# Kernel tuning notes

Hardware: AMD Instinct MI355X
Metric: run time of the kernel (lower is better)

## Reference

```python
import jax, jax.numpy as jnp
import numpy as np

N_LEVELS = 7
N_HEADS = 2
HIDDEN = 128
LP_P = 4.0  # LPPool1d norm


def setup_inputs() -> dict:
    key = jax.random.key(0)
    ks = jax.random.split(key, 9)
    B, S, H = 2048, 200, HIDDEN
    item_seq = jax.random.randint(ks[0], (B, S), 0, 100)
    item_seq_emb = jax.random.normal(ks[1], (B, S, H), dtype=jnp.float32)
    item_seq_len = jax.random.randint(ks[2], (B,), 0, S)
    scale = 0.02
    W_lq = jax.random.normal(ks[3], (H, H), dtype=jnp.float32) * scale
    b_lq = jnp.zeros((H,), dtype=jnp.float32)
    Wq = jax.random.normal(ks[4], (H, H), dtype=jnp.float32) * scale
    bq = jnp.zeros((H,), dtype=jnp.float32)
    Wk = jax.random.normal(ks[5], (H, H), dtype=jnp.float32) * scale
    bk = jnp.zeros((H,), dtype=jnp.float32)
    return {"item_seq": item_seq, "item_seq_emb": item_seq_emb,
            "item_seq_len": item_seq_len, "W_lq": W_lq, "b_lq": b_lq,
            "Wq": Wq, "bq": bq, "Wk": Wk, "bk": bk}


def reference(item_seq, item_seq_emb, item_seq_len, W_lq, b_lq, Wq, bq, Wk, bk):
    B, S, H = item_seq_emb.shape
    nh, L = N_HEADS, N_LEVELS
    d = H // nh
    mask = item_seq > 0  # [B,S]

    # multi-level gather of last j+1 positions; torch clamp(-1) + index -1 == last pos
    j = jnp.arange(L)
    idx = jnp.clip(item_seq_len[:, None] - (j[None, :] + 1), -1, 1000)  # [B,L]
    idx = jnp.where(idx < 0, idx + S, idx)
    gathered = jnp.take_along_axis(item_seq_emb, idx[:, :, None], axis=1)  # [B,L,H]
    level_emb = jnp.cumsum(gathered, axis=1)  # level i = sum of gathers 0..i

    # shared level-query linear (ModuleList([lin]*L) aliases one Linear)
    queries = level_emb @ W_lq.T + b_lq  # [B,L,H]

    # raw torch .view() reshapes replicated exactly
    q = (queries @ Wq.T + bq).reshape(B * nh, L, d)
    k = (item_seq_emb @ Wk.T + bk).reshape(B * nh, S, d)
    v = item_seq_emb.reshape(B, S, nh, d)

    alpha = jax.nn.sigmoid(jnp.einsum('bld,bsd->bls', q, k))  # [B*nh, L, S]
    alpha = alpha.reshape(B, nh * L, S).transpose(0, 2, 1)  # [B, S, nh*L]
    alpha = jax.nn.softmax(alpha, axis=1)

    # LPPool1d(p=4, kernel=L, stride=L) over last dim -> [B,S,nh]
    alpha = alpha.reshape(B, S, nh, L)
    alpha = jnp.sum(alpha ** LP_P, axis=-1) ** (1.0 / LP_P)

    alpha = jnp.where(mask[:, :, None], alpha, -jnp.inf)
    alpha = jax.nn.softmax(alpha, axis=1)  # dropout off (inference)

    weighted = (alpha[..., None] * v).reshape(B, S, H) * mask[:, :, None].astype(item_seq_emb.dtype)
    return jnp.sum(weighted, axis=1)  # [B,H]
```

## Files before the change

### kernel.cpp

```cpp
#include <hip/hip_runtime.h>
#include <hip/hip_bf16.h>

#define SEQ 200
#define HID 128
#define NLVL 7

#define WS_M16_W 0
#define WS_BF    32768
#define WS_VB    33280
#define WS_CB    33792
#define WS_WC    33796
#define WS_BC    50180
#define WS_WORDS 50308

typedef __attribute__((ext_vector_type(8))) short short8;
typedef __attribute__((ext_vector_type(4))) float f32x4;

__device__ __forceinline__ float bf_lo(unsigned u) { return __uint_as_float(u << 16); }
__device__ __forceinline__ float bf_hi(unsigned u) { return __uint_as_float(u & 0xffff0000u); }
__device__ __forceinline__ unsigned short bf_bits(float f) {
    __hip_bfloat16 h = __float2bfloat16(f);
    return *reinterpret_cast<unsigned short*>(&h);
}
__device__ __forceinline__ unsigned pack_bf(float a, float b) {
    return (unsigned)bf_bits(a) | ((unsigned)bf_bits(b) << 16);
}

__global__ __launch_bounds__(256) void precomp0(
    const float* __restrict__ Wlq, const float* __restrict__ blq,
    const float* __restrict__ Wq,  const float* __restrict__ bq,
    float* __restrict__ ws)
{
    int id = blockIdx.x * 256 + threadIdx.x;
    int r = id >> 7, j = id & 127;
    float acc = 0.f;
    #pragma unroll 8
    for (int c = 0; c < 128; ++c) acc += Wq[r * 128 + c] * Wlq[c * 128 + j];
    ws[WS_WC + id] = acc;
    if (id < 128) {
        float b = bq[id];
        #pragma unroll 8
        for (int c = 0; c < 128; ++c) b += Wq[id * 128 + c] * blq[c];
        ws[WS_BC + id] = b;
    }
}

__global__ __launch_bounds__(256) void precomp1(
    const float* __restrict__ Wk, const float* __restrict__ bk, float* __restrict__ ws)
{
    int gid = blockIdx.x * 256 + threadIdx.x;
    if (gid < 65536) {
        int j = gid & 127, c = (gid >> 7) & 127, g = gid >> 14;
        int u = g >> 1, par = g & 1;
        const float* wc = ws + WS_WC + u * 64 * 128 + j;
        const float* wk = Wk + par * 64 * 128 + c;
        float acc = 0.f;
        #pragma unroll 8
        for (int d = 0; d < 64; ++d) acc += wc[d * 128] * wk[d * 128];
        ((__hip_bfloat16*)ws)[gid] = __float2bfloat16(acc);
    } else if (gid < 66048) {
        int t = gid - 65536, c = t & 127, g = t >> 7;
        int u = g >> 1, par = g & 1;
        float acc = 0.f;
        #pragma unroll 8
        for (int d = 0; d < 64; ++d)
            acc += ws[WS_BC + u * 64 + d] * Wk[(par * 64 + d) * 128 + c];
        ws[WS_BF + t] = acc;
    } else if (gid < 66560) {
        int t = gid - 66048, j = t & 127, g = t >> 7;
        int u = g >> 1, par = g & 1;
        float acc = 0.f;
        #pragma unroll 8
        for (int d = 0; d < 64; ++d)
            acc += ws[WS_WC + (u * 64 + d) * 128 + j] * bk[par * 64 + d];
        ws[WS_VB + t] = acc;
    } else if (gid < 66564) {
        int g = gid - 66560, u = g >> 1, par = g & 1;
        float acc = 0.f;
        for (int d = 0; d < 64; ++d)
            acc += ws[WS_BC + u * 64 + d] * bk[par * 64 + d];
        ws[WS_CB + g] = acc;
    }
}

__global__ __launch_bounds__(512, 8) void mixer_main(
    const int* __restrict__ item_seq,
    const float* __restrict__ emb,
    const int* __restrict__ seq_len,
    const float* __restrict__ ws,
    float* __restrict__ out)
{
    const int b    = blockIdx.x;
    const int tid  = threadIdx.x;
    const int wave = tid >> 6, lane = tid & 63;

    __shared__ __align__(16) short s_qkhi[30 * 136];
    __shared__ __align__(16) short s_qklo[30 * 136];
    __shared__ __align__(16) char  s_region[14 * 208 * 4];
    __shared__ float s_qb[28];
    __shared__ float s_rinv[14];
    __shared__ __align__(16) float s_A[2 * SEQ];
    __shared__ __align__(16) float s_red[512];

    float* s_scores = (float*)s_region;
    float* s_lvl    = (float*)s_region;
    short* s_lvl16  = (short*)(s_region + 3584);

    const float* embb = emb + (size_t)b * SEQ * HID;

    if (tid < HID) {
        const int len = seq_len[b];
        float e[NLVL];
        #pragma unroll
        for (int j = 0; j < NLVL; ++j) {
            int idx = len - (j + 1);
            if (idx < 0) idx = SEQ - 1;
            e[j] = embb[(size_t)idx * HID + tid];
        }
        float acc = 0.f;
        #pragma unroll
        for (int j = 0; j < NLVL; ++j) {
            acc += e[j];
            s_lvl[j * HID + tid] = acc;
            s_lvl16[j * 136 + tid] = (short)bf_bits(acc);
        }
    } else if (tid < 196) {
        int t = tid - 128;
        ((uint2*)(s_qkhi + 28 * 136))[t] = make_uint2(0u, 0u);
        ((uint2*)(s_qklo + 28 * 136))[t] = make_uint2(0u, 0u);
    }
    __syncthreads();

    {
        const int g = wave >> 1, halfm = wave & 1;
        const int mrow = lane & 15, quad = lane >> 4;
        short8 bfrag[4];
        #pragma unroll
        for (int k = 0; k < 4; ++k)
            bfrag[k] = *(const short8*)(s_lvl16 + mrow * 136 + k * 32 + quad * 8);
        const short* M16 = (const short*)ws;
        #pragma unroll
        for (int mt = 0; mt < 4; ++mt) {
            int mtile = halfm * 4 + mt;
            int cbase = mtile * 16 + quad * 4;
            f32x4 acc;
            #pragma unroll
            for (int r = 0; r < 4; ++r) acc[r] = ws[WS_BF + g * 128 + cbase + r];
            const short* Ab = M16 + (g * 128 + mtile * 16 + mrow) * 128;
            #pragma unroll
            for (int k = 0; k < 4; ++k) {
                short8 afrag = *(const short8*)(Ab + k * 32 + quad * 8);
                acc = __builtin_amdgcn_mfma_f32_16x16x32_bf16(afrag, bfrag[k], acc, 0, 0, 0);
            }
            if (mrow < NLVL) {
                int qrow = mrow * 4 + g;
                unsigned h01 = pack_bf(acc[0], acc[1]);
                unsigned h23 = pack_bf(acc[2], acc[3]);
                float l0 = acc[0] - bf_lo(h01), l1 = acc[1] - bf_hi(h01);
                float l2 = acc[2] - bf_lo(h23), l3 = acc[3] - bf_hi(h23);
                *(uint2*)(s_qkhi + qrow * 136 + cbase) = make_uint2(h01, h23);
                *(uint2*)(s_qklo + qrow * 136 + cbase) = make_uint2(pack_bf(l0, l1), pack_bf(l2, l3));
            }
        }
        if (tid < 28) {
            int qrow = tid, gg = qrow & 3, L = qrow >> 2;
            const float* vb = ws + WS_VB + gg * 128;
            const float* lv = s_lvl + L * 128;
            float acc = ws[WS_CB + gg];
            #pragma unroll 8
            for (int j = 0; j < 128; ++j) acc += lv[j] * vb[j];
            s_qb[qrow] = acc;
        }
    }
    __syncthreads();

    {
        const int ln = lane & 15, quad = lane >> 4;
        #pragma unroll 1
        for (int t = wave; t < 14; t += 8) {
            const int h = t / 7, mtile = t % 7;
            int gqrow = mtile * 16 + ln;
            int rowg = h * 100 + (gqrow < 100 ? gqrow : 99);
            const float* Arow = embb + (size_t)rowg * HID;
            float qbv = (ln < 14) ? s_qb[h * 14 + ln] : 0.f;
            f32x4 acc;
            acc[0] = qbv; acc[1] = qbv; acc[2] = qbv; acc[3] = qbv;
            #pragma unroll 2
            for (int kk = 0; kk < 4; ++kk) {
                float4 v0 = *(const float4*)(Arow + kk * 32 + quad * 8);
                float4 v1 = *(const float4*)(Arow + kk * 32 + quad * 8 + 4);
                short8 afrag;
                afrag[0] = (short)bf_bits(v0.x); afrag[1] = (short)bf_bits(v0.y);
                afrag[2] = (short)bf_bits(v0.z); afrag[3] = (short)bf_bits(v0.w);
                afrag[4] = (short)bf_bits(v1.x); afrag[5] = (short)bf_bits(v1.y);
                afrag[6] = (short)bf_bits(v1.z); afrag[7] = (short)bf_bits(v1.w);
                const int boff = (h * 14 + ln) * 136 + kk * 32 + quad * 8;
                short8 bhi = *(const short8*)(s_qkhi + boff);
                short8 blo = *(const short8*)(s_qklo + boff);
                acc = __builtin_amdgcn_mfma_f32_16x16x32_bf16(afrag, bhi, acc, 0, 0, 0);
                acc = __builtin_amdgcn_mfma_f32_16x16x32_bf16(afrag, blo, acc, 0, 0, 0);
            }
            if (ln < 14) {
                int srow = (h * 7 + (ln >> 1)) * 208;
                int par = ln & 1;
                #pragma unroll
                for (int i = 0; i < 4; ++i) {
                    int gq = mtile * 16 + quad * 4 + i;
                    if (gq < 100)
                        s_scores[srow + 2 * gq + par] = 1.f / (1.f + __expf(-acc[i]));
                }
            }
        }
    }
    __syncthreads();

    for (int rr = wave; rr < 14; rr += 8) {
        const float* row = s_scores + rr * 208;
        float e0 = __expf(row[lane]);
        float e1 = __expf(row[lane + 64]);
        float e2 = __expf(row[lane + 128]);
        float e3 = (lane + 192 < 200) ? __expf(row[lane + 192]) : 0.f;
        float sum = e0 + e1 + e2 + e3;
        #pragma unroll
        for (int mm = 1; mm < 64; mm <<= 1) sum += __shfl_xor(sum, mm, 64);
        if (lane == 0) s_rinv[rr] = 1.f / sum;
    }
    __syncthreads();

    if (tid < 2 * SEQ) {
        int h = tid / SEQ, s2 = tid % SEQ;
        float ssum = 0.f;
        #pragma unroll
        for (int l = 0; l < NLVL; ++l) {
            float v = __expf(s_scores[(h * NLVL + l) * 208 + s2]) * s_rinv[h * NLVL + l];
            float v2 = v * v;
            ssum += v2 * v2;
        }
        float A = sqrtf(sqrtf(ssum));
        int m = item_seq[(size_t)b * SEQ + s2];
        s_A[tid] = (m > 0) ? __expf(A) : 0.f;
    }
    __syncthreads();

    {
        int c = tid & 127, qq = tid >> 7;
        int h = c >> 6;
        const float* wv = s_A + h * SEQ + qq * 50;
        const float* eg = embb + (size_t)(qq * 50) * HID + c;
        float acc = 0.f;
        #pragma unroll 10
        for (int s = 0; s < 50; ++s)
            acc += wv[s] * eg[(size_t)s * HID];
        s_red[tid] = acc;
    }
    __syncthreads();

    if (tid < HID) {
        int h = tid >> 6;
        const float* row = s_A + h * SEQ;
        float sum = row[lane] + row[lane + 64] + row[lane + 128]
                  + ((lane + 192 < 200) ? row[lane + 192] : 0.f);
        #pragma unroll
        for (int mm = 1; mm < 64; mm <<= 1) sum += __shfl_xor(sum, mm, 64);
        float inv = 1.f / sum;
        float tot = (s_red[tid] + s_red[tid + 128] + s_red[tid + 256] + s_red[tid + 384]) * inv;
        out[(size_t)b * HID + tid] = tot;
    }
}

__global__ __launch_bounds__(256) void mixer_fallback(
    const int* __restrict__ item_seq, const float* __restrict__ emb,
    const int* __restrict__ seq_len,
    const float* __restrict__ Wlq, const float* __restrict__ blq,
    const float* __restrict__ Wq,  const float* __restrict__ bq,
    const float* __restrict__ Wk,  const float* __restrict__ bk,
    float* __restrict__ out)
{
    const int b = blockIdx.x, tid = threadIdx.x;
    __shared__ unsigned s_embu[SEQ * 65];
    __shared__ float s_qk[28 * 128];
    __shared__ float s_qb[28];
    __shared__ float s_tmp[2800];
    __shared__ float s_A[400];
    __shared__ float s_red[256];
    __shared__ float s_inv[2];

    {
        const float4* src = (const float4*)(emb + (size_t)b * SEQ * HID);
        for (int i = tid; i < SEQ * 32; i += 256) {
            int row = i >> 5, j = i & 31;
            float4 v = src[i];
            unsigned* dst = s_embu + row * 65 + 2 * j;
            dst[0] = pack_bf(v.x, v.y);
            dst[1] = pack_bf(v.z, v.w);
        }
    }
    const int len = seq_len[b];
    if (tid < HID) {
        float acc = 0.f;
        for (int j = 0; j < NLVL; ++j) {
            int idx = len - (j + 1);
            if (idx < 0) idx = SEQ - 1;
            acc += emb[(size_t)b * SEQ * HID + (size_t)idx * HID + tid];
            s_tmp[j * HID + tid] = acc;
        }
    }
    __syncthreads();
    for (int t = tid; t < NLVL * HID; t += 256) {
        int l = t >> 7, c = t & 127;
        const float* x = s_tmp + l * HID;
        float acc = blq[c];
        #pragma unroll 8
        for (int k = 0; k < HID; ++k) acc += x[k] * Wlq[c * HID + k];
        s_tmp[896 + t] = acc;
    }
    __syncthreads();
    for (int t = tid; t < NLVL * HID; t += 256) {
        int l = t >> 7, c = t & 127;
        const float* x = s_tmp + 896 + l * HID;
        float acc = bq[c];
        #pragma unroll 8
        for (int k = 0; k < HID; ++k) acc += x[k] * Wq[c * HID + k];
        s_tmp[t] = acc;
    }
    __syncthreads();
    for (int o = tid; o < 28 * 128; o += 256) {
        int qrow = o >> 7, c = o & 127;
        int hl = qrow >> 1, par = qrow & 1;
        const float* qv = s_tmp + hl * 64;
        float acc = 0.f;
        #pragma unroll 8
        for (int d2 = 0; d2 < 64; ++d2) acc += qv[d2] * Wk[(par * 64 + d2) * HID + c];
        s_qk[qrow * 128 + c] = acc;
    }
    if (tid < 28) {
        int hl = tid >> 1, par = tid & 1;
        float acc = 0.f;
        for (int d2 = 0; d2 < 64; ++d2) acc += s_tmp[hl * 64 + d2] * bk[par * 64 + d2];
        s_qb[tid] = acc;
    }
    __syncthreads();
    for (int o = tid; o < 700; o += 256) {
        int hl = o / 50, g = o % 50;
        int h = (hl >= 7) ? 1 : 0;
        int rA = h * 100 + g, rB = rA + 50;
        const unsigned* eA = s_embu + rA * 65;
        const unsigned* eB = s_embu + rB * 65;
        const float* k0 = s_qk + (hl * 2) * 128;
        const float* k1 = s_qk + (hl * 2 + 1) * 128;
        float a0 = 0.f, a1 = 0.f, c0a = 0.f, c1a = 0.f;
        #pragma unroll 4
        for (int kk = 0; kk < 64; ++kk) {
            unsigned uA = eA[kk], uB = eB[kk];
            float2 w0 = *(const float2*)(k0 + 2 * kk);
            float2 w1 = *(const float2*)(k1 + 2 * kk);
            float alo = bf_lo(uA), ahi = bf_hi(uA);
            float blo = bf_lo(uB), bhi = bf_hi(uB);
            a0 += alo * w0.x + ahi * w0.y;  a1 += alo * w1.x + ahi * w1.y;
            c0a += blo * w0.x + bhi * w0.y; c1a += blo * w1.x + bhi * w1.y;
        }
        float qb0 = s_qb[hl * 2], qb1 = s_qb[hl * 2 + 1];
        float* row = s_tmp + hl * 200;
        row[2 * g]       = 1.f / (1.f + __expf(-(a0 + qb0)));
        row[2 * g + 1]   = 1.f / (1.f + __expf(-(a1 + qb1)));
        row[2 * g + 100] = 1.f / (1.f + __expf(-(c0a + qb0)));
        row[2 * g + 101] = 1.f / (1.f + __expf(-(c1a + qb1)));
    }
    __syncthreads();
    const int wave = tid >> 6, lane = tid & 63;
    for (int r = wave; r < 14; r += 4) {
        float* row = s_tmp + r * 200;
        float e0 = __expf(row[lane]), e1 = __expf(row[lane + 64]);
        float e2 = __expf(row[lane + 128]);
        float e3 = (lane + 192 < 200) ? __expf(row[lane + 192]) : 0.f;
        float sum = e0 + e1 + e2 + e3;
        #pragma unroll
        for (int m = 1; m < 64; m <<= 1) sum += __shfl_xor(sum, m, 64);
        float inv = 1.f / sum;
        row[lane] = e0 * inv; row[lane + 64] = e1 * inv; row[lane + 128] = e2 * inv;
        if (lane + 192 < 200) row[lane + 192] = e3 * inv;
    }
    __syncthreads();
    for (int o = tid; o < 2 * SEQ; o += 256) {
        int h = o / SEQ, s2 = o % SEQ;
        float ssum = 0.f;
        #pragma unroll
        for (int l = 0; l < NLVL; ++l) {
            float v = s_tmp[(h * NLVL + l) * 200 + s2];
            float v2 = v * v; ssum += v2 * v2;
        }
        float A = sqrtf(sqrtf(ssum));
        s_A[o] = (item_seq[(size_t)b * SEQ + s2] > 0) ? __expf(A) : 0.f;
    }
    __syncthreads();
    if (wave < 2) {
        const float* row = s_A + wave * SEQ;
        float sum = row[lane] + row[lane + 64] + row[lane + 128]
                  + ((lane + 192 < 200) ? row[lane + 192] : 0.f);
        #pragma unroll
        for (int m = 1; m < 64; m <<= 1) sum += __shfl_xor(sum, m, 64);
        if (lane == 0) s_inv[wave] = 1.f / sum;
    }
    __syncthreads();
    {
        int c = tid & 127, halfb = tid >> 7;
        int h = c >> 6;
        const float* wv = s_A + h * SEQ + halfb * 100;
        float acc = 0.f;
        #pragma unroll 4
        for (int s2 = 0; s2 < 100; ++s2) {
            unsigned u = s_embu[(halfb * 100 + s2) * 65 + (c >> 1)];
            acc += wv[s2] * ((c & 1) ? bf_hi(u) : bf_lo(u));
        }
        s_red[tid] = acc;
    }
    __syncthreads();
    if (tid < HID) {
        int h = tid >> 6;
        out[(size_t)b * HID + tid] = (s_red[tid] + s_red[tid + 128]) * s_inv[h];
    }
}

extern "C" void kernel_launch(void* const* d_in, const int* in_sizes, int n_in,
                              void* d_out, int out_size, void* d_ws, size_t ws_size,
                              hipStream_t stream) {
    const int* item_seq = (const int*)d_in[0];
    const float* emb    = (const float*)d_in[1];
    const int* seq_len  = (const int*)d_in[2];
    const float* Wlq    = (const float*)d_in[3];
    const float* blq    = (const float*)d_in[4];
    const float* Wq     = (const float*)d_in[5];
    const float* bq     = (const float*)d_in[6];
    const float* Wk     = (const float*)d_in[7];
    const float* bk     = (const float*)d_in[8];
    float* out          = (float*)d_out;
    const int B = in_sizes[2];

    if (ws_size >= (size_t)WS_WORDS * 4) {
        float* ws = (float*)d_ws;
        precomp0<<<64, 256, 0, stream>>>(Wlq, blq, Wq, bq, ws);
        precomp1<<<261, 256, 0, stream>>>(Wk, bk, ws);
        mixer_main<<<B, 512, 0, stream>>>(item_seq, emb, seq_len, ws, out);
    } else {
        mixer_fallback<<<B, 256, 0, stream>>>(item_seq, emb, seq_len, Wlq, blq, Wq, bq, Wk, bk, out);
    }
}
```

Baseline: 358.8 us.

## Prefetch score-GEMM embedding tiles before query projection to overlap global loads

The embedding rows for each wave's score-tile MFMA are now loaded from global memory and converted to bf16 at kernel start, before the first barrier. This hides that load latency behind the level gather and query-projection phases. The tile loop is replaced by at most two statically assigned tiles held in registers. The score row stride changes from 208 to 212 to alter LDS bank mapping, and launch bounds drop from 8 to 6 waves per EU. The extra live registers may lower occupancy.

```diff
diff --git a/kernel.cpp b/kernel.cpp
--- a/kernel.cpp
+++ b/kernel.cpp
@@ -12,6 +12,8 @@
 #define WS_WC    33796
 #define WS_BC    50180
 #define WS_WORDS 50308
+
+#define SCST 212
 
 typedef __attribute__((ext_vector_type(8))) short short8;
 typedef __attribute__((ext_vector_type(4))) float f32x4;
@@ -83,7 +85,7 @@
     }
 }
 
-__global__ __launch_bounds__(512, 8) void mixer_main(
+__global__ __launch_bounds__(512, 6) void mixer_main(
     const int* __restrict__ item_seq,
     const float* __restrict__ emb,
     const int* __restrict__ seq_len,
@@ -93,10 +95,11 @@
     const int b    = blockIdx.x;
     const int tid  = threadIdx.x;
     const int wave = tid >> 6, lane = tid & 63;
+    const int ln   = lane & 15, quad = lane >> 4;
 
     __shared__ __align__(16) short s_qkhi[30 * 136];
     __shared__ __align__(16) short s_qklo[30 * 136];
-    __shared__ __align__(16) char  s_region[14 * 208 * 4];
+    __shared__ __align__(16) char  s_region[14 * SCST * 4];
     __shared__ float s_qb[28];
     __shared__ float s_rinv[14];
     __shared__ __align__(16) float s_A[2 * SEQ];
@@ -108,8 +111,25 @@
 
     const float* embb = emb + (size_t)b * SEQ * HID;
 
+    const int t0 = wave;
+    const int t1 = (wave >= 2) ? wave + 6 : -1;
+
+    const int len = seq_len[b];
+
+    float4 p[8];
+    {
+        const int h = t0 / 7, m = t0 % 7;
+        int gq = m * 16 + ln;
+        int rowg = h * 100 + (gq < 100 ? gq : 99);
+        const float* Ar = embb + (size_t)rowg * HID + quad * 8;
+        #pragma unroll
+        for (int kk = 0; kk < 4; ++kk) {
+            p[2 * kk]     = *(const float4*)(Ar + kk * 32);
+            p[2 * kk + 1] = *(const float4*)(Ar + kk * 32 + 4);
+        }
+    }
+
     if (tid < HID) {
-        const int len = seq_len[b];
         float e[NLVL];
         #pragma unroll
         for (int j = 0; j < NLVL; ++j) {
@@ -129,11 +149,42 @@
         ((uint2*)(s_qkhi + 28 * 136))[t] = make_uint2(0u, 0u);
         ((uint2*)(s_qklo + 28 * 136))[t] = make_uint2(0u, 0u);
     }
+
+    short8 a0[4], a1[4];
+    #pragma unroll
+    for (int kk = 0; kk < 4; ++kk) {
+        short8 f;
+        f[0] = (short)bf_bits(p[2*kk].x); f[1] = (short)bf_bits(p[2*kk].y);
+        f[2] = (short)bf_bits(p[2*kk].z); f[3] = (short)bf_bits(p[2*kk].w);
+        f[4] = (short)bf_bits(p[2*kk+1].x); f[5] = (short)bf_bits(p[2*kk+1].y);
+        f[6] = (short)bf_bits(p[2*kk+1].z); f[7] = (short)bf_bits(p[2*kk+1].w);
+        a0[kk] = f;
+    }
+    if (t1 >= 0) {
+        const int h = t1 / 7, m = t1 % 7;
+        int gq = m * 16 + ln;
+        int rowg = h * 100 + (gq < 100 ? gq : 99);
+        const float* Ar = embb + (size_t)rowg * HID + quad * 8;
+        #pragma unroll
+        for (int kk = 0; kk < 4; ++kk) {
+            p[2 * kk]     = *(const float4*)(Ar + kk * 32);
+            p[2 * kk + 1] = *(const float4*)(Ar + kk * 32 + 4);
+        }
+        #pragma unroll
+        for (int kk = 0; kk < 4; ++kk) {
+            short8 f;
+            f[0] = (short)bf_bits(p[2*kk].x); f[1] = (short)bf_bits(p[2*kk].y);
+            f[2] = (short)bf_bits(p[2*kk].z); f[3] = (short)bf_bits(p[2*kk].w);
+            f[4] = (short)bf_bits(p[2*kk+1].x); f[5] = (short)bf_bits(p[2*kk+1].y);
+            f[6] = (short)bf_bits(p[2*kk+1].z); f[7] = (short)bf_bits(p[2*kk+1].w);
+            a1[kk] = f;
+        }
+    }
     __syncthreads();
 
     {
         const int g = wave >> 1, halfm = wave & 1;
-        const int mrow = lane & 15, quad = lane >> 4;
+        const int mrow = ln;
         short8 bfrag[4];
         #pragma unroll
         for (int k = 0; k < 4; ++k)
@@ -174,48 +225,38 @@
     }
     __syncthreads();
 
-    {
-        const int ln = lane & 15, quad = lane >> 4;
-        #pragma unroll 1
-        for (int t = wave; t < 14; t += 8) {
-            const int h = t / 7, mtile = t % 7;
-            int gqrow = mtile * 16 + ln;
-            int rowg = h * 100 + (gqrow < 100 ? gqrow : 99);
-            const float* Arow = embb + (size_t)rowg * HID;
-            float qbv = (ln < 14) ? s_qb[h * 14 + ln] : 0.f;
-            f32x4 acc;
-            acc[0] = qbv; acc[1] = qbv; acc[2] = qbv; acc[3] = qbv;
-            #pragma unroll 2
-            for (int kk = 0; kk < 4; ++kk) {
-                float4 v0 = *(const float4*)(Arow + kk * 32 + quad * 8);
-                float4 v1 = *(const float4*)(Arow + kk * 32 + quad * 8 + 4);
-                short8 afrag;
-                afrag[0] = (short)bf_bits(v0.x); afrag[1] = (short)bf_bits(v0.y);
-                afrag[2] = (short)bf_bits(v0.z); afrag[3] = (short)bf_bits(v0.w);
-                afrag[4] = (short)bf_bits(v1.x); afrag[5] = (short)bf_bits(v1.y);
-                afrag[6] = (short)bf_bits(v1.z); afrag[7] = (short)bf_bits(v1.w);
-                const int boff = (h * 14 + ln) * 136 + kk * 32 + quad * 8;
-                short8 bhi = *(const short8*)(s_qkhi + boff);
-                short8 blo = *(const short8*)(s_qklo + boff);
-                acc = __builtin_amdgcn_mfma_f32_16x16x32_bf16(afrag, bhi, acc, 0, 0, 0);
-                acc = __builtin_amdgcn_mfma_f32_16x16x32_bf16(afrag, blo, acc, 0, 0, 0);
+    #pragma unroll
+    for (int which = 0; which < 2; ++which) {
+        const int t = (which == 0) ? t0 : t1;
+        if (t < 0) continue;
+        const int h = t / 7, mtile = t % 7;
+        const short8* af = (which == 0) ? a0 : a1;
+        float qbv = (ln < 14) ? s_qb[h * 14 + ln] : 0.f;
+        f32x4 acc;
+        acc[0] = qbv; acc[1] = qbv; acc[2] = qbv; acc[3] = qbv;
+        #pragma unroll
+        for (int kk = 0; kk < 4; ++kk) {
+            const int boff = (h * 14 + ln) * 136 + kk * 32 + quad * 8;
+            short8 bhi = *(const short8*)(s_qkhi + boff);
+            short8 blo = *(const short8*)(s_qklo + boff);
+            acc = __builtin_amdgcn_mfma_f32_16x16x32_bf16(af[kk], bhi, acc, 0, 0, 0);
+            acc = __builtin_amdgcn_mfma_f32_16x16x32_bf16(af[kk], blo, acc, 0, 0, 0);
+        }
+        if (ln < 14) {
+            int srow = (h * 7 + (ln >> 1)) * SCST;
+            int par = ln & 1;
+            #pragma unroll
+            for (int i = 0; i < 4; ++i) {
+                int gq = mtile * 16 + quad * 4 + i;
+                if (gq < 100)
+                    s_scores[srow + 2 * gq + par] = 1.f / (1.f + __expf(-acc[i]));
             }
-            if (ln < 14) {
-                int srow = (h * 7 + (ln >> 1)) * 208;
-                int par = ln & 1;
-                #pragma unroll
-                for (int i = 0; i < 4; ++i) {
-                    int gq = mtile * 16 + quad * 4 + i;
-                    if (gq < 100)
-                        s_scores[srow + 2 * gq + par] = 1.f / (1.f + __expf(-acc[i]));
-                }
-            }
         }
     }
     __syncthreads();
 
     for (int rr = wave; rr < 14; rr += 8) {
-        const float* row = s_scores + rr * 208;
+        const float* row = s_scores + rr * SCST;
         float e0 = __expf(row[lane]);
         float e1 = __expf(row[lane + 64]);
         float e2 = __expf(row[lane + 128]);
@@ -232,7 +273,7 @@
         float ssum = 0.f;
         #pragma unroll
         for (int l = 0; l < NLVL; ++l) {
-            float v = __expf(s_scores[(h * NLVL + l) * 208 + s2]) * s_rinv[h * NLVL + l];
+            float v = __expf(s_scores[(h * NLVL + l) * SCST + s2]) * s_rinv[h * NLVL + l];
             float v2 = v * v;
             ssum += v2 * v2;
         }
```

New measurement: 391.8 us. 1.09x slower.

## Prefetch score-GEMM rows early, fuse softmax denominators into score epilogue

Applied to the files above, without the earlier changes.

Each wave now loads and converts its first embedding tile for the score MFMA before the level/query stage and its barrier, hiding global latency behind that work. The second score tile is issued early and unrolled. The softmax row sums are accumulated during the sigmoid epilogue with shuffles and LDS atomics, which removes a separate reduction pass and one barrier. The per-level query-bias dot product is split across 16 lanes with shuffle reduction. The score stride is padded to 212. The cost is higher register pressure and LDS atomic contention on the denominators.

```diff
diff --git a/kernel.cpp b/kernel.cpp
--- a/kernel.cpp
+++ b/kernel.cpp
@@ -13,6 +13,8 @@
 #define WS_BC    50180
 #define WS_WORDS 50308
 
+#define SCST 212
+
 typedef __attribute__((ext_vector_type(8))) short short8;
 typedef __attribute__((ext_vector_type(4))) float f32x4;
 
@@ -24,6 +26,14 @@
 }
 __device__ __forceinline__ unsigned pack_bf(float a, float b) {
     return (unsigned)bf_bits(a) | ((unsigned)bf_bits(b) << 16);
+}
+__device__ __forceinline__ short8 cvt8(float4 a, float4 b) {
+    short8 f;
+    f[0] = (short)bf_bits(a.x); f[1] = (short)bf_bits(a.y);
+    f[2] = (short)bf_bits(a.z); f[3] = (short)bf_bits(a.w);
+    f[4] = (short)bf_bits(b.x); f[5] = (short)bf_bits(b.y);
+    f[6] = (short)bf_bits(b.z); f[7] = (short)bf_bits(b.w);
+    return f;
 }
 
 __global__ __launch_bounds__(256) void precomp0(
@@ -93,12 +103,13 @@
     const int b    = blockIdx.x;
     const int tid  = threadIdx.x;
     const int wave = tid >> 6, lane = tid & 63;
+    const int ln   = lane & 15, quad = lane >> 4;
 
     __shared__ __align__(16) short s_qkhi[30 * 136];
     __shared__ __align__(16) short s_qklo[30 * 136];
-    __shared__ __align__(16) char  s_region[14 * 208 * 4];
+    __shared__ __align__(16) char  s_region[14 * SCST * 4];
     __shared__ float s_qb[28];
-    __shared__ float s_rinv[14];
+    __shared__ float s_denom[14];
     __shared__ __align__(16) float s_A[2 * SEQ];
     __shared__ __align__(16) float s_red[512];
 
@@ -108,8 +119,25 @@
 
     const float* embb = emb + (size_t)b * SEQ * HID;
 
+    const int len = seq_len[b];
+
+    const int hA = wave / 7, mA = wave % 7;
+    const float* Ar0;
+    {
+        int gq = mA * 16 + ln;
+        int rowg = hA * 100 + (gq < 100 ? gq : 99);
+        Ar0 = embb + (size_t)rowg * HID + quad * 8;
+    }
+    float4 q0 = *(const float4*)(Ar0);
+    float4 q1 = *(const float4*)(Ar0 + 4);
+    float4 q2 = *(const float4*)(Ar0 + 32);
+    float4 q3 = *(const float4*)(Ar0 + 36);
+    float4 q4 = *(const float4*)(Ar0 + 64);
+    float4 q5 = *(const float4*)(Ar0 + 68);
+    float4 q6 = *(const float4*)(Ar0 + 96);
+    float4 q7 = *(const float4*)(Ar0 + 100);
+
     if (tid < HID) {
-        const int len = seq_len[b];
         float e[NLVL];
         #pragma unroll
         for (int j = 0; j < NLVL; ++j) {
@@ -128,12 +156,19 @@
         int t = tid - 128;
         ((uint2*)(s_qkhi + 28 * 136))[t] = make_uint2(0u, 0u);
         ((uint2*)(s_qklo + 28 * 136))[t] = make_uint2(0u, 0u);
-    }
+    } else if (tid < 210) {
+        s_denom[tid - 196] = 0.f;
+    }
+
+    short8 a00 = cvt8(q0, q1);
+    short8 a01 = cvt8(q2, q3);
+    short8 a02 = cvt8(q4, q5);
+    short8 a03 = cvt8(q6, q7);
     __syncthreads();
 
     {
         const int g = wave >> 1, halfm = wave & 1;
-        const int mrow = lane & 15, quad = lane >> 4;
+        const int mrow = ln;
         short8 bfrag[4];
         #pragma unroll
         for (int k = 0; k < 4; ++k)
@@ -162,68 +197,110 @@
                 *(uint2*)(s_qklo + qrow * 136 + cbase) = make_uint2(pack_bf(l0, l1), pack_bf(l2, l3));
             }
         }
-        if (tid < 28) {
-            int qrow = tid, gg = qrow & 3, L = qrow >> 2;
+        if (tid < 448) {
+            int grp = tid >> 4, sub = tid & 15;
+            int gg = grp & 3, L = grp >> 2;
             const float* vb = ws + WS_VB + gg * 128;
             const float* lv = s_lvl + L * 128;
-            float acc = ws[WS_CB + gg];
-            #pragma unroll 8
-            for (int j = 0; j < 128; ++j) acc += lv[j] * vb[j];
-            s_qb[qrow] = acc;
+            float acc = 0.f;
+            #pragma unroll
+            for (int k = 0; k < 8; ++k) {
+                int j = sub + 16 * k;
+                acc += lv[j] * vb[j];
+            }
+            acc += __shfl_xor(acc, 1, 16);
+            acc += __shfl_xor(acc, 2, 16);
+            acc += __shfl_xor(acc, 4, 16);
+            acc += __shfl_xor(acc, 8, 16);
+            if (sub == 0) s_qb[grp] = acc + ws[WS_CB + gg];
         }
     }
     __syncthreads();
 
     {
-        const int ln = lane & 15, quad = lane >> 4;
-        #pragma unroll 1
-        for (int t = wave; t < 14; t += 8) {
-            const int h = t / 7, mtile = t % 7;
-            int gqrow = mtile * 16 + ln;
-            int rowg = h * 100 + (gqrow < 100 ? gqrow : 99);
-            const float* Arow = embb + (size_t)rowg * HID;
-            float qbv = (ln < 14) ? s_qb[h * 14 + ln] : 0.f;
+        const bool hasB = (wave < 6);
+        const int mB = wave + 1;
+        const float* ArB = embb;
+        float4 r0, r1, r2, r3;
+        if (hasB) {
+            int gq = mB * 16 + ln;
+            int rowg = 100 + (gq < 100 ? gq : 99);
+            ArB = embb + (size_t)rowg * HID + quad * 8;
+            r0 = *(const float4*)(ArB);
+            r1 = *(const float4*)(ArB + 4);
+            r2 = *(const float4*)(ArB + 32);
+            r3 = *(const float4*)(ArB + 36);
+        }
+        {
+            float qbv = (ln < 14) ? s_qb[hA * 14 + ln] : 0.f;
             f32x4 acc;
             acc[0] = qbv; acc[1] = qbv; acc[2] = qbv; acc[3] = qbv;
-            #pragma unroll 2
-            for (int kk = 0; kk < 4; ++kk) {
-                float4 v0 = *(const float4*)(Arow + kk * 32 + quad * 8);
-                float4 v1 = *(const float4*)(Arow + kk * 32 + quad * 8 + 4);
-                short8 afrag;
-                afrag[0] = (short)bf_bits(v0.x); afrag[1] = (short)bf_bits(v0.y);
-                afrag[2] = (short)bf_bits(v0.z); afrag[3] = (short)bf_bits(v0.w);
-                afrag[4] = (short)bf_bits(v1.x); afrag[5] = (short)bf_bits(v1.y);
-                afrag[6] = (short)bf_bits(v1.z); afrag[7] = (short)bf_bits(v1.w);
-                const int boff = (h * 14 + ln) * 136 + kk * 32 + quad * 8;
-                short8 bhi = *(const short8*)(s_qkhi + boff);
-                short8 blo = *(const short8*)(s_qklo + boff);
-                acc = __builtin_amdgcn_mfma_f32_16x16x32_bf16(afrag, bhi, acc, 0, 0, 0);
-                acc = __builtin_amdgcn_mfma_f32_16x16x32_bf16(afrag, blo, acc, 0, 0, 0);
-            }
+            const int bb = (hA * 14 + ln) * 136 + quad * 8;
+            acc = __builtin_amdgcn_mfma_f32_16x16x32_bf16(a00, *(const short8*)(s_qkhi + bb), acc, 0, 0, 0);
+            acc = __builtin_amdgcn_mfma_f32_16x16x32_bf16(a00, *(const short8*)(s_qklo + bb), acc, 0, 0, 0);
+            acc = __builtin_amdgcn_mfma_f32_16x16x32_bf16(a01, *(const short8*)(s_qkhi + bb + 32), acc, 0, 0, 0);
+            acc = __builtin_amdgcn_mfma_f32_16x16x32_bf16(a01, *(const short8*)(s_qklo + bb + 32), acc, 0, 0, 0);
+            acc = __builtin_amdgcn_mfma_f32_16x16x32_bf16(a02, *(const short8*)(s_qkhi + bb + 64), acc, 0, 0, 0);
+            acc = __builtin_amdgcn_mfma_f32_16x16x32_bf16(a02, *(const short8*)(s_qklo + bb + 64), acc, 0, 0, 0);
+            acc = __builtin_amdgcn_mfma_f32_16x16x32_bf16(a03, *(const short8*)(s_qkhi + bb + 96), acc, 0, 0, 0);
+            acc = __builtin_amdgcn_mfma_f32_16x16x32_bf16(a03, *(const short8*)(s_qklo + bb + 96), acc, 0, 0, 0);
+            float part = 0.f;
             if (ln < 14) {
-                int srow = (h * 7 + (ln >> 1)) * 208;
-                int par = ln & 1;
+                int srow = (hA * 7 + (ln >> 1)) * SCST, par = ln & 1;
                 #pragma unroll
                 for (int i = 0; i < 4; ++i) {
-                    int gq = mtile * 16 + quad * 4 + i;
-                    if (gq < 100)
-                        s_scores[srow + 2 * gq + par] = 1.f / (1.f + __expf(-acc[i]));
+                    int gq = mA * 16 + quad * 4 + i;
+                    if (gq < 100) {
+                        float sg = 1.f / (1.f + __expf(-acc[i]));
+                        s_scores[srow + 2 * gq + par] = sg;
+                        part += __expf(sg);
+                    }
                 }
             }
-        }
-    }
-    __syncthreads();
-
-    for (int rr = wave; rr < 14; rr += 8) {
-        const float* row = s_scores + rr * 208;
-        float e0 = __expf(row[lane]);
-        float e1 = __expf(row[lane + 64]);
-        float e2 = __expf(row[lane + 128]);
-        float e3 = (lane + 192 < 200) ? __expf(row[lane + 192]) : 0.f;
-        float sum = e0 + e1 + e2 + e3;
-        #pragma unroll
-        for (int mm = 1; mm < 64; mm <<= 1) sum += __shfl_xor(sum, mm, 64);
-        if (lane == 0) s_rinv[rr] = 1.f / sum;
+            part += __shfl_xor(part, 16, 64);
+            part += __shfl_xor(part, 32, 64);
+            if (ln < 14 && quad == 0)
+                atomicAdd(&s_denom[hA * 7 + (ln >> 1)], part);
+        }
+        if (hasB) {
+            short8 b0 = cvt8(r0, r1);
+            short8 b1 = cvt8(r2, r3);
+            float4 r4 = *(const float4*)(ArB + 64);
+            float4 r5 = *(const float4*)(ArB + 68);
+            float4 r6 = *(const float4*)(ArB + 96);
+            float4 r7 = *(const float4*)(ArB + 100);
+            float qbv = (ln < 14) ? s_qb[14 + ln] : 0.f;
+            f32x4 acc;
+            acc[0] = qbv; acc[1] = qbv; acc[2] = qbv; acc[3] = qbv;
+            const int bb = (14 + ln) * 136 + quad * 8;
+            acc = __builtin_amdgcn_mfma_f32_16x16x32_bf16(b0, *(const short8*)(s_qkhi + bb), acc, 0, 0, 0);
+            acc = __builtin_amdgcn_mfma_f32_16x16x32_bf16(b0, *(const short8*)(s_qklo + bb), acc, 0, 0, 0);
+            acc = __builtin_amdgcn_mfma_f32_16x16x32_bf16(b1, *(const short8*)(s_qkhi + bb + 32), acc, 0, 0, 0);
+            acc = __builtin_amdgcn_mfma_f32_16x16x32_bf16(b1, *(const short8*)(s_qklo + bb + 32), acc, 0, 0, 0);
+            short8 b2 = cvt8(r4, r5);
+            short8 b3 = cvt8(r6, r7);
+            acc = __builtin_amdgcn_mfma_f32_16x16x32_bf16(b2, *(const short8*)(s_qkhi + bb + 64), acc, 0, 0, 0);
+            acc = __builtin_amdgcn_mfma_f32_16x16x32_bf16(b2, *(const short8*)(s_qklo + bb + 64), acc, 0, 0, 0);
+            acc = __builtin_amdgcn_mfma_f32_16x16x32_bf16(b3, *(const short8*)(s_qkhi + bb + 96), acc, 0, 0, 0);
+            acc = __builtin_amdgcn_mfma_f32_16x16x32_bf16(b3, *(const short8*)(s_qklo + bb + 96), acc, 0, 0, 0);
+            float part = 0.f;
+            if (ln < 14) {
+                int srow = (7 + (ln >> 1)) * SCST, par = ln & 1;
+                #pragma unroll
+                for (int i = 0; i < 4; ++i) {
+                    int gq = mB * 16 + quad * 4 + i;
+                    if (gq < 100) {
+                        float sg = 1.f / (1.f + __expf(-acc[i]));
+                        s_scores[srow + 2 * gq + par] = sg;
+                        part += __expf(sg);
+                    }
+                }
+            }
+            part += __shfl_xor(part, 16, 64);
+            part += __shfl_xor(part, 32, 64);
+            if (ln < 14 && quad == 0)
+                atomicAdd(&s_denom[7 + (ln >> 1)], part);
+        }
     }
     __syncthreads();
 
@@ -232,7 +309,8 @@
         float ssum = 0.f;
         #pragma unroll
         for (int l = 0; l < NLVL; ++l) {
-            float v = __expf(s_scores[(h * NLVL + l) * 208 + s2]) * s_rinv[h * NLVL + l];
+            float v = __fdividef(__expf(s_scores[(h * NLVL + l) * SCST + s2]),
+                                 s_denom[h * NLVL + l]);
             float v2 = v * v;
             ssum += v2 * v2;
         }
```

New measurement: 364.1 us. Within noise of the previous version (+1.5%).

## Split per-batch query projection into separate kernel and fuse softmax exp into scoring

Applied to the files above, without the earlier changes.

Moves the per-batch level gather and query/key-combined projection into a new precomp2 kernel that writes hi/lo bf16 query tiles and biases to workspace, which mixer_main then bulk-copies into LDS. The exponent for the first softmax is now computed in the score epilogue, with row sums accumulated through shared atomics instead of a separate reduction pass. This is meant to shorten the main kernel's serial prologue and drop one barrier-delimited phase. In exchange it adds a kernel launch, a global round trip of about 16KB per batch, and requires a much larger workspace, falling back to the slow path otherwise.

```diff
diff --git a/kernel.cpp b/kernel.cpp
--- a/kernel.cpp
+++ b/kernel.cpp
@@ -13,6 +13,11 @@
 #define WS_BC    50180
 #define WS_WORDS 50308
 
+#define WS_QK    51200
+#define QK_STRIDE 4112
+
+#define SCST 212
+
 typedef __attribute__((ext_vector_type(8))) short short8;
 typedef __attribute__((ext_vector_type(4))) float f32x4;
 
@@ -24,6 +29,14 @@
 }
 __device__ __forceinline__ unsigned pack_bf(float a, float b) {
     return (unsigned)bf_bits(a) | ((unsigned)bf_bits(b) << 16);
+}
+__device__ __forceinline__ short8 cvt8(float4 a, float4 b) {
+    short8 f;
+    f[0] = (short)bf_bits(a.x); f[1] = (short)bf_bits(a.y);
+    f[2] = (short)bf_bits(a.z); f[3] = (short)bf_bits(a.w);
+    f[4] = (short)bf_bits(b.x); f[5] = (short)bf_bits(b.y);
+    f[6] = (short)bf_bits(b.z); f[7] = (short)bf_bits(b.w);
+    return f;
 }
 
 __global__ __launch_bounds__(256) void precomp0(
@@ -83,33 +96,23 @@
     }
 }
 
-__global__ __launch_bounds__(512, 8) void mixer_main(
-    const int* __restrict__ item_seq,
-    const float* __restrict__ emb,
-    const int* __restrict__ seq_len,
-    const float* __restrict__ ws,
-    float* __restrict__ out)
+__global__ __launch_bounds__(512, 8) void precomp2(
+    const float* __restrict__ emb, const int* __restrict__ seq_len,
+    float* __restrict__ ws)
 {
     const int b    = blockIdx.x;
     const int tid  = threadIdx.x;
     const int wave = tid >> 6, lane = tid & 63;
-
-    __shared__ __align__(16) short s_qkhi[30 * 136];
-    __shared__ __align__(16) short s_qklo[30 * 136];
-    __shared__ __align__(16) char  s_region[14 * 208 * 4];
-    __shared__ float s_qb[28];
-    __shared__ float s_rinv[14];
-    __shared__ __align__(16) float s_A[2 * SEQ];
-    __shared__ __align__(16) float s_red[512];
-
-    float* s_scores = (float*)s_region;
-    float* s_lvl    = (float*)s_region;
-    short* s_lvl16  = (short*)(s_region + 3584);
-
+    const int ln   = lane & 15, quad = lane >> 4;
+
+    __shared__ __align__(16) float s_lvl[NLVL * 128];
+    __shared__ __align__(16) short s_lvl16[16 * 136];
+
+    unsigned* wq = (unsigned*)ws + WS_QK + (size_t)b * QK_STRIDE;
     const float* embb = emb + (size_t)b * SEQ * HID;
+    const int len = seq_len[b];
 
     if (tid < HID) {
-        const int len = seq_len[b];
         float e[NLVL];
         #pragma unroll
         for (int j = 0; j < NLVL; ++j) {
@@ -124,16 +127,18 @@
             s_lvl[j * HID + tid] = acc;
             s_lvl16[j * 136 + tid] = (short)bf_bits(acc);
         }
-    } else if (tid < 196) {
-        int t = tid - 128;
-        ((uint2*)(s_qkhi + 28 * 136))[t] = make_uint2(0u, 0u);
-        ((uint2*)(s_qklo + 28 * 136))[t] = make_uint2(0u, 0u);
+    } else if (tid >= 448) {
+        int t = tid - 448;
+        for (int i = t; i < 136; i += 64) {
+            wq[1904 + i] = 0u;
+            wq[3944 + i] = 0u;
+        }
     }
     __syncthreads();
 
     {
         const int g = wave >> 1, halfm = wave & 1;
-        const int mrow = lane & 15, quad = lane >> 4;
+        const int mrow = ln;
         short8 bfrag[4];
         #pragma unroll
         for (int k = 0; k < 4; ++k)
@@ -158,24 +163,63 @@
                 unsigned h23 = pack_bf(acc[2], acc[3]);
                 float l0 = acc[0] - bf_lo(h01), l1 = acc[1] - bf_hi(h01);
                 float l2 = acc[2] - bf_lo(h23), l3 = acc[3] - bf_hi(h23);
-                *(uint2*)(s_qkhi + qrow * 136 + cbase) = make_uint2(h01, h23);
-                *(uint2*)(s_qklo + qrow * 136 + cbase) = make_uint2(pack_bf(l0, l1), pack_bf(l2, l3));
+                int woff = qrow * 68 + mtile * 8 + quad * 2;
+                *(uint2*)(wq + woff)        = make_uint2(h01, h23);
+                *(uint2*)(wq + 2040 + woff) = make_uint2(pack_bf(l0, l1), pack_bf(l2, l3));
             }
         }
-        if (tid < 28) {
-            int qrow = tid, gg = qrow & 3, L = qrow >> 2;
+        if (tid < 448) {
+            int grp = tid >> 4, sub = tid & 15;
+            int gg = grp & 3, L = grp >> 2;
             const float* vb = ws + WS_VB + gg * 128;
             const float* lv = s_lvl + L * 128;
-            float acc = ws[WS_CB + gg];
-            #pragma unroll 8
-            for (int j = 0; j < 128; ++j) acc += lv[j] * vb[j];
-            s_qb[qrow] = acc;
-        }
-    }
-    __syncthreads();
-
-    {
-        const int ln = lane & 15, quad = lane >> 4;
+            float acc = 0.f;
+            #pragma unroll
+            for (int k = 0; k < 8; ++k) {
+                int j = sub + 16 * k;
+                acc += lv[j] * vb[j];
+            }
+            acc += __shfl_xor(acc, 1, 16);
+            acc += __shfl_xor(acc, 2, 16);
+            acc += __shfl_xor(acc, 4, 16);
+            acc += __shfl_xor(acc, 8, 16);
+            if (sub == 0) ((float*)(wq + 4080))[grp] = acc + ws[WS_CB + gg];
+        }
+    }
+}
+
+__global__ __launch_bounds__(512, 8) void mixer_main(
+    const int* __restrict__ item_seq,
+    const float* __restrict__ emb,
+    const float* __restrict__ ws,
+    float* __restrict__ out)
+{
+    const int b    = blockIdx.x;
+    const int tid  = threadIdx.x;
+    const int wave = tid >> 6, lane = tid & 63;
+    const int ln   = lane & 15, quad = lane >> 4;
+
+    __shared__ __align__(16) unsigned s_qkbuf[4108];
+    __shared__ __align__(16) float s_scores[14 * SCST];
+    __shared__ float s_denom[14];
+    __shared__ __align__(16) float s_A[2 * SEQ];
+    __shared__ __align__(16) float s_red[512];
+
+    short* s_qkhi = (short*)s_qkbuf;
+    float* s_qb   = (float*)(s_qkbuf + 4080);
+
+    const float* embb = emb + (size_t)b * SEQ * HID;
+    const unsigned* qsrc = (const unsigned*)ws + WS_QK + (size_t)b * QK_STRIDE;
+
+    {
+        const uint4* src = (const uint4*)qsrc;
+        uint4* dst = (uint4*)s_qkbuf;
+        for (int i = tid; i < 1027; i += 512) dst[i] = src[i];
+        if (tid < 14) s_denom[tid] = 0.f;
+    }
+    __syncthreads();
+
+    {
         #pragma unroll 1
         for (int t = wave; t < 14; t += 8) {
             const int h = t / 7, mtile = t % 7;
@@ -189,41 +233,33 @@
             for (int kk = 0; kk < 4; ++kk) {
                 float4 v0 = *(const float4*)(Arow + kk * 32 + quad * 8);
                 float4 v1 = *(const float4*)(Arow + kk * 32 + quad * 8 + 4);
-                short8 afrag;
-                afrag[0] = (short)bf_bits(v0.x); afrag[1] = (short)bf_bits(v0.y);
-                afrag[2] = (short)bf_bits(v0.z); afrag[3] = (short)bf_bits(v0.w);
-                afrag[4] = (short)bf_bits(v1.x); afrag[5] = (short)bf_bits(v1.y);
-                afrag[6] = (short)bf_bits(v1.z); afrag[7] = (short)bf_bits(v1.w);
+                short8 afrag = cvt8(v0, v1);
                 const int boff = (h * 14 + ln) * 136 + kk * 32 + quad * 8;
                 short8 bhi = *(const short8*)(s_qkhi + boff);
-                short8 blo = *(const short8*)(s_qklo + boff);
+                short8 blo = *(const short8*)(s_qkhi + 2040 * 2 + boff);
                 acc = __builtin_amdgcn_mfma_f32_16x16x32_bf16(afrag, bhi, acc, 0, 0, 0);
                 acc = __builtin_amdgcn_mfma_f32_16x16x32_bf16(afrag, blo, acc, 0, 0, 0);
             }
+            float part = 0.f;
             if (ln < 14) {
-                int srow = (h * 7 + (ln >> 1)) * 208;
-                int par = ln & 1;
+                int srow = (h * 7 + (ln >> 1)) * SCST, par = ln & 1;
                 #pragma unroll
                 for (int i = 0; i < 4; ++i) {
                     int gq = mtile * 16 + quad * 4 + i;
-                    if (gq < 100)
-                        s_scores[srow + 2 * gq + par] = 1.f / (1.f + __expf(-acc[i]));
+                    if (gq < 100) {
+                        float sg = 1.f / (1.f + __expf(-acc[i]));
+                        float E = __expf(sg);
+                        s_scores[srow + 2 * gq + par] = E;
+                        part += E;
+                    }
                 }
             }
-        }
-    }
-    __syncthreads();
-
-    for (int rr = wave; rr < 14; rr += 8) {
-        const float* row = s_scores + rr * 208;
-        float e0 = __expf(row[lane]);
-        float e1 = __expf(row[lane + 64]);
-        float e2 = __expf(row[lane + 128]);
-        float e3 = (lane + 192 < 200) ? __expf(row[lane + 192]) : 0.f;
-        float sum = e0 + e1 + e2 + e3;
-        #pragma unroll
-        for (int mm = 1; mm < 64; mm <<= 1) sum += __shfl_xor(sum, mm, 64);
-        if (lane == 0) s_rinv[rr] = 1.f / sum;
+            part += __shfl_xor(part, 16, 64);
+            part += __shfl_xor(part, 32, 64);
+            part += __shfl_xor(part, 1, 64);
+            if (quad == 0 && ln < 14 && (ln & 1) == 0)
+                atomicAdd(&s_denom[h * 7 + (ln >> 1)], part);
+        }
     }
     __syncthreads();
 
@@ -232,7 +268,8 @@
         float ssum = 0.f;
         #pragma unroll
         for (int l = 0; l < NLVL; ++l) {
-            float v = __expf(s_scores[(h * NLVL + l) * 208 + s2]) * s_rinv[h * NLVL + l];
+            float v = __fdividef(s_scores[(h * NLVL + l) * SCST + s2],
+                                 s_denom[h * NLVL + l]);
             float v2 = v * v;
             ssum += v2 * v2;
         }
@@ -436,11 +473,13 @@
     float* out          = (float*)d_out;
     const int B = in_sizes[2];
 
-    if (ws_size >= (size_t)WS_WORDS * 4) {
+    const size_t need = ((size_t)WS_QK + (size_t)B * QK_STRIDE) * 4;
+    if (ws_size >= need) {
         float* ws = (float*)d_ws;
         precomp0<<<64, 256, 0, stream>>>(Wlq, blq, Wq, bq, ws);
         precomp1<<<261, 256, 0, stream>>>(Wk, bk, ws);
-        mixer_main<<<B, 512, 0, stream>>>(item_seq, emb, seq_len, ws, out);
+        precomp2<<<B, 512, 0, stream>>>(emb, seq_len, ws);
+        mixer_main<<<B, 512, 0, stream>>>(item_seq, emb, ws, out);
     } else {
         mixer_fallback<<<B, 256, 0, stream>>>(item_seq, emb, seq_len, Wlq, blq, Wq, bq, Wk, bk, out);
     }
```

Result: slower. 370.4 us (+3.2%).
